# Performance work log

Hardware: AMD Instinct MI355X
Metric: run time of the kernel (lower is better)

## Reference

```python
import math
import jax, jax.numpy as jnp
import numpy as np

B, T, D = 4, 4096, 512


def setup_inputs() -> dict:
    key = jax.random.key(0)
    k1, _ = jax.random.split(key)
    x = jax.random.normal(k1, (B, T, D), dtype=jnp.float32)
    log_alpha = jnp.zeros((), dtype=jnp.float32)
    return {"x": x, "log_alpha": log_alpha}


def _gelu_tanh(x):
    c = math.sqrt(2.0 / math.pi)
    return 0.5 * x * (1.0 + jnp.tanh(c * (x + 0.044715 * x * x * x)))


def reference(x, log_alpha):
    Bx, Tx, Dx = x.shape
    alpha = jax.nn.softplus(log_alpha)
    # F.normalize(dim=-1): x / max(||x||, eps)
    norm = jnp.maximum(jnp.linalg.norm(x, axis=-1, keepdims=True), 1e-12)
    x_norm = x / norm
    sim = jnp.einsum("btd,bsd->bts", x_norm, x_norm)  # [B,T,T]
    # causal mask: triu incl. diagonal (col >= row) filled with -2.0
    row = jnp.arange(Tx)[:, None]
    col = jnp.arange(Tx)[None, :]
    mask = col >= row  # [T,T]
    sim = jnp.where(mask[None], jnp.float32(-2.0), sim)
    max_sim = jnp.max(sim, axis=-1)  # [B,T]
    max_sim = jnp.maximum(max_sim, -1.0)
    familiarity = (max_sim + 1.0) * 0.5
    novelty = 1.0 - familiarity
    gate = 1.0 + alpha * novelty[..., None]  # [B,T,1]
    return _gelu_tanh(x * gate)
```

## Files before the change

kernel.cpp:

```cpp
#include <hip/hip_runtime.h>
#include <hip/hip_bf16.h>
#include <math.h>

#define B_ 4
#define T_ 4096
#define D_ 512
#define BT 128
#define BK 32
#define NT (T_ / BT)
#define NPAIR (NT * (NT + 1) / 2)


typedef short bf16x8 __attribute__((ext_vector_type(8)));
typedef float f32x4 __attribute__((ext_vector_type(4)));

__device__ __forceinline__ unsigned short f2bf(float f) {
    unsigned u = __float_as_uint(f);
    u += 0x7FFFu + ((u >> 16) & 1u);
    return (unsigned short)(u >> 16);
}
__device__ __forceinline__ unsigned f2ord(float f) {
    unsigned u = __float_as_uint(f);
    return (u & 0x80000000u) ? ~u : (u | 0x80000000u);
}
__device__ __forceinline__ float ord2f(unsigned u) {
    unsigned b = (u & 0x80000000u) ? (u ^ 0x80000000u) : ~u;
    return __uint_as_float(b);
}

__device__ __forceinline__ void async16(const unsigned short* g, unsigned short* l) {
    __builtin_amdgcn_global_load_lds(
        (const __attribute__((address_space(1))) unsigned int*)g,
        (__attribute__((address_space(3))) unsigned int*)l, 16, 0, 0);
}

__global__ __launch_bounds__(256) void k_norm(const float* __restrict__ x,
                                              unsigned short* __restrict__ xn,
                                              unsigned* __restrict__ maxsim) {
    int w = (blockIdx.x * 256 + threadIdx.x) >> 6;
    int lane = threadIdx.x & 63;
    const float4* xr = (const float4*)(x + (size_t)w * D_);
    float4 a = xr[lane];
    float4 b = xr[lane + 64];
    float ss = a.x * a.x + a.y * a.y + a.z * a.z + a.w * a.w +
               b.x * b.x + b.y * b.y + b.z * b.z + b.w * b.w;
#pragma unroll
    for (int off = 32; off > 0; off >>= 1) ss += __shfl_xor(ss, off);
    float inv = 1.0f / fmaxf(sqrtf(ss), 1e-12f);
    unsigned u0 = (unsigned)f2bf(a.x * inv) | ((unsigned)f2bf(a.y * inv) << 16);
    unsigned u1 = (unsigned)f2bf(a.z * inv) | ((unsigned)f2bf(a.w * inv) << 16);
    unsigned u2 = (unsigned)f2bf(b.x * inv) | ((unsigned)f2bf(b.y * inv) << 16);
    unsigned u3 = (unsigned)f2bf(b.z * inv) | ((unsigned)f2bf(b.w * inv) << 16);
    uint2* xo = (uint2*)(xn + (size_t)w * D_);
    xo[lane]      = make_uint2(u0, u1);
    xo[lane + 64] = make_uint2(u2, u3);
    if (lane == 0) maxsim[w] = f2ord(-2.0f);
}

__global__ __launch_bounds__(256, 4) void k_maxsim(const unsigned short* __restrict__ xn,
                                                   unsigned* __restrict__ maxsim) {
    __shared__ __align__(16) unsigned short As[BT * BK];
    __shared__ __align__(16) unsigned short Bs[BT * BK];
    const int b = blockIdx.y;
    const int p = blockIdx.x;
    int ti = (int)((sqrtf(8.0f * (float)p + 1.0f) - 1.0f) * 0.5f);
    while ((ti + 1) * (ti + 2) / 2 <= p) ti++;
    while (ti * (ti + 1) / 2 > p) ti--;
    const int si = p - ti * (ti + 1) / 2;
    const int t0 = ti * BT, s0 = si * BT;

    const int tid = threadIdx.x;
    const int wave = tid >> 6, lane = tid & 63;
    const int wm = wave >> 1, wn = wave & 1;
    const int qa = lane >> 4, la = lane & 15;
    const int swz = (la >> 1) & 3;

    const unsigned short* Ab = xn + (size_t)(b * T_ + t0) * D_;
    const unsigned short* Bb = xn + (size_t)(b * T_ + s0) * D_;

    f32x4 acc[4][4];
#pragma unroll
    for (int i = 0; i < 4; i++)
#pragma unroll
        for (int j = 0; j < 4; j++) acc[i][j] = (f32x4){0.f, 0.f, 0.f, 0.f};

    for (int k0 = 0; k0 < D_; k0 += BK) {
#pragma unroll
        for (int j = 0; j < 2; j++) {
            int c = j * 256 + tid;
            int row = c >> 2;
            int chunk = (c & 3) ^ ((row >> 1) & 3);
            int ldsbase = (j * 256 + wave * 64) * 8;
            async16(Ab + (size_t)row * D_ + k0 + chunk * 8, &As[ldsbase]);
            async16(Bb + (size_t)row * D_ + k0 + chunk * 8, &Bs[ldsbase]);
        }
        __syncthreads();
        bf16x8 af[4], bfr[4];
#pragma unroll
        for (int i = 0; i < 4; i++)
            af[i] = *(const bf16x8*)&As[(wm * 64 + i * 16 + la) * BK + (qa ^ swz) * 8];
#pragma unroll
        for (int j = 0; j < 4; j++)
            bfr[j] = *(const bf16x8*)&Bs[(wn * 64 + j * 16 + la) * BK + (qa ^ swz) * 8];
#pragma unroll
        for (int i = 0; i < 4; i++)
#pragma unroll
            for (int j = 0; j < 4; j++)
                acc[i][j] = __builtin_amdgcn_mfma_f32_16x16x32_bf16(af[i], bfr[j], acc[i][j], 0, 0, 0);
        __syncthreads();
    }

    const bool diag = (ti == si);
#pragma unroll
    for (int i = 0; i < 4; i++) {
#pragma unroll
        for (int r = 0; r < 4; r++) {
            int tl = wm * 64 + i * 16 + qa * 4 + r;
            float m = -2.0f;
#pragma unroll
            for (int j = 0; j < 4; j++) {
                int sl = wn * 64 + j * 16 + la;
                float v = acc[i][j][r];
                if (!diag || sl < tl) m = fmaxf(m, v);
            }
#pragma unroll
            for (int off = 1; off < 16; off <<= 1) m = fmaxf(m, __shfl_xor(m, off));
            if (la == 0) atomicMax(&maxsim[b * T_ + t0 + tl], f2ord(m));
        }
    }
}

__device__ __forceinline__ float gelu_tanh(float y) {
    float t = tanhf(0.7978845608028654f * (y + 0.044715f * y * y * y));
    return 0.5f * y * (1.0f + t);
}

__global__ __launch_bounds__(256) void k_gate(const float* __restrict__ x,
                                              const float* __restrict__ log_alpha,
                                              const unsigned* __restrict__ maxsim,
                                              float* __restrict__ out) {
    int idx = blockIdx.x * 256 + threadIdx.x;
    float la = log_alpha[0];
    float alpha = (la > 20.0f) ? la : log1pf(expf(la));
    int row = idx >> 7;
    float m = fmaxf(ord2f(maxsim[row]), -1.0f);
    float novelty = 1.0f - (m + 1.0f) * 0.5f;
    float gate = 1.0f + alpha * novelty;
    float4 v = ((const float4*)x)[idx];
    float4 o;
    o.x = gelu_tanh(v.x * gate);
    o.y = gelu_tanh(v.y * gate);
    o.z = gelu_tanh(v.z * gate);
    o.w = gelu_tanh(v.w * gate);
    ((float4*)out)[idx] = o;
}

extern "C" void kernel_launch(void* const* d_in, const int* in_sizes, int n_in,
                              void* d_out, int out_size, void* d_ws, size_t ws_size,
                              hipStream_t stream) {
    const float* x = (const float*)d_in[0];
    const float* log_alpha = (const float*)d_in[1];
    float* out = (float*)d_out;

    unsigned* maxsim = (unsigned*)d_ws;
    unsigned short* xn = (unsigned short*)((char*)d_ws + 65536);

    const int rows = B_ * T_;
    k_norm<<<rows / 4, 256, 0, stream>>>(x, xn, maxsim);

    dim3 g2(NPAIR, B_);
    k_maxsim<<<g2, 256, 0, stream>>>(xn, maxsim);

    k_gate<<<(B_ * T_ * D_ / 4) / 256, 256, 0, stream>>>(x, log_alpha, maxsim, out);
}
```

Measured before the change: 158.8 us.

## Restructure maxsim GEMM into single-wave 64x128 tiles with double-buffered async loads

The similarity max kernel now uses one 64-thread wave per block computing a 64x128 tile, with a new triangular pair mapping that skips more of the masked upper region. K-steps are double-buffered in LDS with global_load_lds prefetch and waitcnt instead of __syncthreads, so loads overlap MFMA. It also changes the LDS swizzle. This raises per-thread accumulators (32 f32x4) and block count, which may cost occupancy or increase atomic traffic.

```diff
diff --git a/kernel.cpp b/kernel.cpp
--- a/kernel.cpp
+++ b/kernel.cpp
@@ -5,10 +5,11 @@
 #define B_ 4
 #define T_ 4096
 #define D_ 512
-#define BT 128
+#define TM 64
+#define TS 128
 #define BK 32
-#define NT (T_ / BT)
-#define NPAIR (NT * (NT + 1) / 2)
+#define STEPS (D_ / BK)
+#define NPAIR 1056
 
 
 typedef short bf16x8 __attribute__((ext_vector_type(8)));
@@ -57,75 +58,92 @@
     if (lane == 0) maxsim[w] = f2ord(-2.0f);
 }
 
-__global__ __launch_bounds__(256, 4) void k_maxsim(const unsigned short* __restrict__ xn,
-                                                   unsigned* __restrict__ maxsim) {
-    __shared__ __align__(16) unsigned short As[BT * BK];
-    __shared__ __align__(16) unsigned short Bs[BT * BK];
+__global__ __launch_bounds__(64) void k_maxsim(const unsigned short* __restrict__ xn,
+                                               unsigned* __restrict__ maxsim) {
+    __shared__ __align__(16) unsigned short Buf[2][6144];
     const int b = blockIdx.y;
     const int p = blockIdx.x;
-    int ti = (int)((sqrtf(8.0f * (float)p + 1.0f) - 1.0f) * 0.5f);
-    while ((ti + 1) * (ti + 2) / 2 <= p) ti++;
-    while (ti * (ti + 1) / 2 > p) ti--;
-    const int si = p - ti * (ti + 1) / 2;
-    const int t0 = ti * BT, s0 = si * BT;
+    int m0 = (int)((sqrtf(4.0f * (float)p + 1.0f) - 1.0f) * 0.5f);
+    while ((m0 + 1) * (m0 + 2) <= p) m0++;
+    while (m0 * (m0 + 1) > p) m0--;
+    int ti = 2 * m0, base = m0 * (m0 + 1);
+    if (p - base > m0) { ti++; base += m0 + 1; }
+    const int sj = p - base;
+    const int t0 = ti * TM, s0 = sj * TS;
 
-    const int tid = threadIdx.x;
-    const int wave = tid >> 6, lane = tid & 63;
-    const int wm = wave >> 1, wn = wave & 1;
-    const int qa = lane >> 4, la = lane & 15;
-    const int swz = (la >> 1) & 3;
+    const int l = threadIdx.x;
+    const int qa = l >> 4, la = l & 15;
 
     const unsigned short* Ab = xn + (size_t)(b * T_ + t0) * D_;
     const unsigned short* Bb = xn + (size_t)(b * T_ + s0) * D_;
 
-    f32x4 acc[4][4];
+    const int ca = (l & 3) ^ ((l >> 2) & 3) ^ ((l >> 4) & 3);
+    const unsigned short* gA = Ab + (size_t)(l >> 2) * D_ + ca * 8;
+    const unsigned short* gB = Bb + (size_t)(l >> 2) * D_ + ca * 8;
+
+    const int pos8 = ((qa ^ (la & 3) ^ ((la >> 2) & 3)) & 3) * 8;
+
+#define STAGE(step, st)                                                      \
+    do {                                                                     \
+        _Pragma("unroll")                                                    \
+        for (int j_ = 0; j_ < 4; j_++)                                       \
+            async16(gA + (size_t)j_ * 16 * D_ + (step) * BK,                 \
+                    &Buf[st][j_ * 512]);                                     \
+        _Pragma("unroll")                                                    \
+        for (int j_ = 0; j_ < 8; j_++)                                       \
+            async16(gB + (size_t)j_ * 16 * D_ + (step) * BK,                 \
+                    &Buf[st][2048 + j_ * 512]);                              \
+    } while (0)
+
+    f32x4 acc[4][8];
 #pragma unroll
     for (int i = 0; i < 4; i++)
 #pragma unroll
-        for (int j = 0; j < 4; j++) acc[i][j] = (f32x4){0.f, 0.f, 0.f, 0.f};
+        for (int j = 0; j < 8; j++) acc[i][j] = (f32x4){0.f, 0.f, 0.f, 0.f};
 
-    for (int k0 = 0; k0 < D_; k0 += BK) {
+    STAGE(0, 0);
+
 #pragma unroll
-        for (int j = 0; j < 2; j++) {
-            int c = j * 256 + tid;
-            int row = c >> 2;
-            int chunk = (c & 3) ^ ((row >> 1) & 3);
-            int ldsbase = (j * 256 + wave * 64) * 8;
-            async16(Ab + (size_t)row * D_ + k0 + chunk * 8, &As[ldsbase]);
-            async16(Bb + (size_t)row * D_ + k0 + chunk * 8, &Bs[ldsbase]);
+    for (int k = 0; k < STEPS; ++k) {
+        if (k + 1 < STEPS) {
+            STAGE(k + 1, (k + 1) & 1);
+            __builtin_amdgcn_s_waitcnt(0x0F7C);
+        } else {
+            __builtin_amdgcn_s_waitcnt(0x0F70);
         }
-        __syncthreads();
-        bf16x8 af[4], bfr[4];
+        __asm__ __volatile__("" ::: "memory");
+
+        const unsigned short* S = &Buf[k & 1][0];
+        bf16x8 af[4], bfr[8];
 #pragma unroll
         for (int i = 0; i < 4; i++)
-            af[i] = *(const bf16x8*)&As[(wm * 64 + i * 16 + la) * BK + (qa ^ swz) * 8];
+            af[i] = *(const bf16x8*)&S[(i * 16 + la) * 32 + pos8];
 #pragma unroll
-        for (int j = 0; j < 4; j++)
-            bfr[j] = *(const bf16x8*)&Bs[(wn * 64 + j * 16 + la) * BK + (qa ^ swz) * 8];
+        for (int j = 0; j < 8; j++)
+            bfr[j] = *(const bf16x8*)&S[2048 + (j * 16 + la) * 32 + pos8];
 #pragma unroll
         for (int i = 0; i < 4; i++)
 #pragma unroll
-            for (int j = 0; j < 4; j++)
+            for (int j = 0; j < 8; j++)
                 acc[i][j] = __builtin_amdgcn_mfma_f32_16x16x32_bf16(af[i], bfr[j], acc[i][j], 0, 0, 0);
-        __syncthreads();
     }
+#undef STAGE
 
-    const bool diag = (ti == si);
 #pragma unroll
     for (int i = 0; i < 4; i++) {
 #pragma unroll
         for (int r = 0; r < 4; r++) {
-            int tl = wm * 64 + i * 16 + qa * 4 + r;
-            float m = -2.0f;
+            int tg = t0 + i * 16 + qa * 4 + r;
+            float mx = -2.0f;
 #pragma unroll
-            for (int j = 0; j < 4; j++) {
-                int sl = wn * 64 + j * 16 + la;
+            for (int j = 0; j < 8; j++) {
+                int sg = s0 + j * 16 + la;
                 float v = acc[i][j][r];
-                if (!diag || sl < tl) m = fmaxf(m, v);
+                if (sg < tg) mx = fmaxf(mx, v);
             }
 #pragma unroll
-            for (int off = 1; off < 16; off <<= 1) m = fmaxf(m, __shfl_xor(m, off));
-            if (la == 0) atomicMax(&maxsim[b * T_ + t0 + tl], f2ord(m));
+            for (int off = 1; off < 16; off <<= 1) mx = fmaxf(mx, __shfl_xor(mx, off));
+            if (la == 0) atomicMax(&maxsim[b * T_ + tg], f2ord(mx));
         }
     }
 }
@@ -169,7 +187,7 @@
     k_norm<<<rows / 4, 256, 0, stream>>>(x, xn, maxsim);
 
     dim3 g2(NPAIR, B_);
-    k_maxsim<<<g2, 256, 0, stream>>>(xn, maxsim);
+    k_maxsim<<<g2, 64, 0, stream>>>(xn, maxsim);
 
     k_gate<<<(B_ * T_ * D_ / 4) / 256, 256, 0, stream>>>(x, log_alpha, maxsim, out);
 }
```

Measured after the change: 159.5 us. About the same (+0.4%).
